# Optimization experiments

Measured on AMD Instinct MI355X. Metric: run time of the kernel, lower is better.

The kernel has to match this reference:

```python
import jax, jax.numpy as jnp
import numpy as np

D_MODEL = 1024
NUM_HEADS = 16
HEAD_DIM = D_MODEL // NUM_HEADS


def setup_inputs() -> dict:
    key = jax.random.key(0)
    ks = jax.random.split(key, 9)
    s = 1.0 / np.sqrt(D_MODEL)
    x = jax.random.normal(ks[0], (2, 2048, D_MODEL), dtype=jnp.float32)
    Wq = jax.random.uniform(ks[1], (D_MODEL, D_MODEL), jnp.float32, -s, s)
    bq = jax.random.uniform(ks[2], (D_MODEL,), jnp.float32, -s, s)
    Wk = jax.random.uniform(ks[3], (D_MODEL, D_MODEL), jnp.float32, -s, s)
    bk = jax.random.uniform(ks[4], (D_MODEL,), jnp.float32, -s, s)
    Wv = jax.random.uniform(ks[5], (D_MODEL, D_MODEL), jnp.float32, -s, s)
    bv = jax.random.uniform(ks[6], (D_MODEL,), jnp.float32, -s, s)
    Wo = jax.random.uniform(ks[7], (D_MODEL, D_MODEL), jnp.float32, -s, s)
    bo = jax.random.uniform(ks[8], (D_MODEL,), jnp.float32, -s, s)
    return {"x": x, "Wq": Wq, "bq": bq, "Wk": Wk, "bk": bk,
            "Wv": Wv, "bv": bv, "Wo": Wo, "bo": bo}


def reference(x, Wq, bq, Wk, bk, Wv, bv, Wo, bo):
    B, S, _ = x.shape
    def split_heads(t):  # [B,S,D] -> [B,H,S,hd]
        return t.reshape(B, S, NUM_HEADS, HEAD_DIM).transpose(0, 2, 1, 3)
    q = split_heads(x @ Wq + bq)
    k = split_heads(x @ Wk + bk)
    v = split_heads(x @ Wv + bv)
    scores = jnp.einsum('bhqd,bhkd->bhqk', q, k) / np.sqrt(HEAD_DIM)
    attn = jax.nn.softmax(scores, axis=-1)
    ctx = jnp.einsum('bhqk,bhkd->bhqd', attn, v)
    ctx = ctx.transpose(0, 2, 1, 3).reshape(B, S, D_MODEL)
    return ctx @ Wo + bo
```

## Files before the change

### kernel.cpp

```cpp
#include <hip/hip_runtime.h>
#include <stdint.h>

#define DM 1024
#define SEQ 2048
#define NTOK 4096
#define HD 64

typedef __bf16 bf16x8 __attribute__((ext_vector_type(8)));
typedef float f32x4 __attribute__((ext_vector_type(4)));
typedef uint32_t u32x2 __attribute__((ext_vector_type(2)));
typedef uint32_t u32x4 __attribute__((ext_vector_type(4)));

#if __has_builtin(__builtin_amdgcn_exp2f)
#define EXP2F(x) __builtin_amdgcn_exp2f(x)
#else
#define EXP2F(x) exp2f(x)
#endif

__device__ __forceinline__ void gll16f(const char* g, char* lds_wave_base, int lane) {
#if __has_builtin(__builtin_amdgcn_global_load_lds)
  __builtin_amdgcn_global_load_lds(
      (const __attribute__((address_space(1))) void*)g,
      (__attribute__((address_space(3))) void*)lds_wave_base, 16, 0, 0);
#else
  *(bf16x8*)(lds_wave_base + lane * 16) = *(const bf16x8*)g;
#endif
}

__device__ __forceinline__ uint16_t f2bf(float f) {
  uint32_t x = __float_as_uint(f);
  return (uint16_t)((x + 0x7fffu + ((x >> 16) & 1u)) >> 16);
}

__device__ __forceinline__ uint32_t cvtpk(float a, float b) {
  uint32_t r;
  asm("v_cvt_pk_bf16_f32 %0, %1, %2" : "=v"(r) : "v"(a), "v"(b));
  return r;
}

__device__ __forceinline__ bf16x8 mk8(uint32_t a, uint32_t b, uint32_t c, uint32_t d) {
  u32x4 t = {a, b, c, d};
  return __builtin_bit_cast(bf16x8, t);
}

__global__ void cvt_x_kernel(const float* __restrict__ x, uint16_t* __restrict__ xb) {
  int i = (blockIdx.x * 256 + threadIdx.x) * 4;
  float4 v = *(const float4*)&x[i];
  uint64_t pk = (uint64_t)f2bf(v.x) | ((uint64_t)f2bf(v.y) << 16) |
                ((uint64_t)f2bf(v.z) << 32) | ((uint64_t)f2bf(v.w) << 48);
  *(uint64_t*)&xb[i] = pk;
}

__global__ void twt4_kernel(const float* __restrict__ W0, const float* __restrict__ W1,
                            const float* __restrict__ W2, const float* __restrict__ W3,
                            uint16_t* __restrict__ T0, uint16_t* __restrict__ T1,
                            uint16_t* __restrict__ T2, uint16_t* __restrict__ T3) {
  __shared__ float t[32][33];
  int z = blockIdx.z;
  const float* W = (z == 0) ? W0 : (z == 1) ? W1 : (z == 2) ? W2 : W3;
  uint16_t* T = (z == 0) ? T0 : (z == 1) ? T1 : (z == 2) ? T2 : T3;
  int tx = threadIdx.x, ty = threadIdx.y;
  int kb = blockIdx.y * 32, nb = blockIdx.x * 32;
#pragma unroll
  for (int i = 0; i < 4; i++)
    t[ty + i * 8][tx] = W[(kb + ty + i * 8) * DM + nb + tx];
  __syncthreads();
#pragma unroll
  for (int i = 0; i < 4; i++)
    T[(nb + ty + i * 8) * DM + kb + tx] = f2bf(t[tx][ty + i * 8]);
}

template <int MODE, int MF>
__device__ __forceinline__ void gemm_body(const uint16_t* __restrict__ A,
                                          const uint16_t* __restrict__ Bt,
                                          const float* __restrict__ bias, float scale,
                                          void* __restrict__ out, uint16_t* lds) {
  const int tid = threadIdx.x;
  const int w = tid >> 6, lane = tid & 63;
  const int wr = w >> 1, wc = w & 1;
  const int a15 = lane & 15, a4 = lane >> 4;
  const int m0 = blockIdx.y * (MF * 32), n0 = blockIdx.x * 128;
  uint16_t* lgA = lds;
  uint16_t* lgB = lds + MF * 1024;
  f32x4 acc[MF][4];
#pragma unroll
  for (int m = 0; m < MF; m++)
#pragma unroll
    for (int n = 0; n < 4; n++) acc[m][n] = (f32x4){0.f, 0.f, 0.f, 0.f};

  const char* Ag = (const char*)(A + (size_t)m0 * DM);
  const char* Bg = (const char*)(Bt + (size_t)n0 * DM);

  for (int k0 = 0; k0 < DM; k0 += 32) {
#pragma unroll
    for (int c = 0; c < MF / 2; c++) {
      int o = w * (MF * 512) + c * 1024 + lane * 16;
      int row = o >> 6, colb = o & 63;
      gll16f(Ag + (size_t)row * (DM * 2) + k0 * 2 + colb,
             (char*)lgA + w * (MF * 512) + c * 1024, lane);
    }
#pragma unroll
    for (int c = 0; c < 2; c++) {
      int o = w * 2048 + c * 1024 + lane * 16;
      int row = o >> 6, colb = o & 63;
      gll16f(Bg + (size_t)row * (DM * 2) + k0 * 2 + colb,
             (char*)lgB + w * 2048 + c * 1024, lane);
    }
    __syncthreads();
    bf16x8 af[MF], bfr[4];
#pragma unroll
    for (int m = 0; m < MF; m++)
      af[m] = *(const bf16x8*)&lgA[(wr * (MF * 16) + m * 16 + a15) * 32 + a4 * 8];
#pragma unroll
    for (int n = 0; n < 4; n++)
      bfr[n] = *(const bf16x8*)&lgB[(wc * 64 + n * 16 + a15) * 32 + a4 * 8];
#pragma unroll
    for (int m = 0; m < MF; m++)
#pragma unroll
      for (int n = 0; n < 4; n++)
        acc[m][n] = __builtin_amdgcn_mfma_f32_16x16x32_bf16(af[m], bfr[n], acc[m][n], 0, 0, 0);
    __syncthreads();
  }

#pragma unroll
  for (int m = 0; m < MF; m++) {
#pragma unroll
    for (int n = 0; n < 4; n++) {
      int gr0 = m0 + wr * (MF * 16) + m * 16 + a4 * 4;
      int col = n0 + wc * 64 + n * 16 + a15;
      float bv = bias[col];
      if constexpr (MODE == 2) {
        float* O = (float*)out;
#pragma unroll
        for (int j = 0; j < 4; j++)
          O[(size_t)(gr0 + j) * DM + col] = acc[m][n][j] + bv;
      } else if constexpr (MODE == 0) {
        uint16_t* O = (uint16_t*)out;
        int h = col >> 6, d = col & 63;
#pragma unroll
        for (int j = 0; j < 4; j++) {
          int gr = gr0 + j;
          int b = gr >> 11, s = gr & 2047;
          O[((size_t)(((b << 4) + h)) * SEQ + s) * HD + d] = f2bf((acc[m][n][j] + bv) * scale);
        }
      } else {
        uint16_t* O = (uint16_t*)out;
        int h = col >> 6, d = col & 63;
        int b = gr0 >> 11, s0 = gr0 & 2047;
        uint64_t pk = 0;
#pragma unroll
        for (int j = 0; j < 4; j++)
          pk |= (uint64_t)f2bf(acc[m][n][j] + bv) << (16 * j);
        *(uint64_t*)&O[((size_t)(((b << 4) + h)) * HD + d) * SEQ + s0] = pk;
      }
    }
  }
}

#define CS_SCALE 0.180336880f

__global__ __launch_bounds__(256, 2) void gemm_qkv_kernel(
    const uint16_t* __restrict__ xb, const uint16_t* __restrict__ wtq,
    const uint16_t* __restrict__ wtk, const uint16_t* __restrict__ wtv,
    const float* __restrict__ bq, const float* __restrict__ bk,
    const float* __restrict__ bv, uint16_t* __restrict__ qo,
    uint16_t* __restrict__ ko, uint16_t* __restrict__ vto) {
  __shared__ __attribute__((aligned(16))) uint16_t lds[2 * 128 * 32];
  int z = blockIdx.z;
  if (z == 0)      gemm_body<0, 4>(xb, wtq, bq, CS_SCALE, qo, lds);
  else if (z == 1) gemm_body<0, 4>(xb, wtk, bk, 1.0f, ko, lds);
  else             gemm_body<1, 4>(xb, wtv, bv, 1.0f, vto, lds);
}

__global__ __launch_bounds__(256, 2) void gemm_out_kernel(
    const uint16_t* __restrict__ ctx, const uint16_t* __restrict__ wto,
    const float* __restrict__ bo, float* __restrict__ out) {
  __shared__ __attribute__((aligned(16))) uint16_t lds[2 * 1024 + 128 * 32];
  gemm_body<2, 2>(ctx, wto, bo, 1.0f, out, lds);
}

__global__ __launch_bounds__(256, 2) void attn_kernel(
    const uint16_t* __restrict__ qg, const uint16_t* __restrict__ kg,
    const uint16_t* __restrict__ vtg, uint16_t* __restrict__ ctx) {
  const int tid = threadIdx.x;
  const int w = tid >> 6, l = tid & 63;
  const int l15 = l & 15, g = l >> 4;
  int id = blockIdx.x;
  int wg = (id & 7) * 64 + (id >> 3);
  int bh = wg >> 4, qb = wg & 15;
  const int q0 = qb * 128 + w * 32;
  const uint16_t* Qb = qg + (size_t)bh * SEQ * HD;
  const char* Kc = (const char*)(kg + (size_t)bh * SEQ * HD);
  const char* Vc = (const char*)(vtg + (size_t)bh * HD * SEQ);

  __shared__ __attribute__((aligned(16))) char Klds[2][8192];
  __shared__ __attribute__((aligned(16))) char Vlds[2][8192];

  const int srow = l >> 3;
  const int scolx = ((l & 7) * 16) ^ (srow << 4);

#define STAGE(BI, IT)                                                          \
  {                                                                            \
    const int it1_ = (IT);                                                     \
    _Pragma("unroll") for (int i = 0; i < 2; i++) {                            \
      int r = w * 16 + i * 8 + srow;                                           \
      gll16f(Kc + (size_t)(it1_ * 64 + r) * 128 + scolx,                       \
             &Klds[BI][w * 2048 + i * 1024], l);                               \
      gll16f(Vc + (size_t)r * (SEQ * 2) + it1_ * 128 + scolx,                  \
             &Vlds[BI][w * 2048 + i * 1024], l);                               \
    }                                                                          \
  }

  bf16x8 bq[2][2];
#pragma unroll
  for (int qs = 0; qs < 2; qs++)
#pragma unroll
    for (int ks = 0; ks < 2; ks++)
      bq[qs][ks] = *(const bf16x8*)&Qb[(size_t)(q0 + qs * 16 + l15) * HD + ks * 32 + g * 8];

  f32x4 o[4][2];
#pragma unroll
  for (int dt = 0; dt < 4; dt++)
#pragma unroll
    for (int qs = 0; qs < 2; qs++) o[dt][qs] = (f32x4){0.f, 0.f, 0.f, 0.f};
  f32x4 ol0 = {0.f, 0.f, 0.f, 0.f}, ol1 = {0.f, 0.f, 0.f, 0.f};
  const int swz = (l15 & 7) << 4;
  const uint32_t ONE2 = 0x3F803F80u;
  const bf16x8 aones = mk8(ONE2, ONE2, ONE2, ONE2);

  STAGE(0, 0);

#define ATTN_TILE(IT, BI, BN)                                                  \
  {                                                                            \
    const int it_ = (IT);                                                      \
    if (it_ + 1 < SEQ / 64) {                                                  \
      STAGE(BN, it_ + 1);                                                      \
      asm volatile("s_waitcnt vmcnt(4)\n\ts_barrier" ::: "memory");            \
    } else {                                                                   \
      asm volatile("s_waitcnt vmcnt(0)\n\ts_barrier" ::: "memory");            \
    }                                                                          \
                                            \
    bf16x8 ak[4][2];                                                           \
    _Pragma("unroll") for (int kt = 0; kt < 4; kt++)                           \
        _Pragma("unroll") for (int ks = 0; ks < 2; ks++)                       \
            ak[kt][ks] = *(const bf16x8*)&Klds[BI][(kt * 16 + l15) * 128 +     \
                                                   ((ks * 64 + g * 16) ^ swz)];\
      \
    bf16x8 av[4][2];                                                           \
    _Pragma("unroll") for (int dt = 0; dt < 4; dt++)                           \
        _Pragma("unroll") for (int kb = 0; kb < 2; kb++) {                     \
      int rb = (dt * 16 + l15) * 128;                                          \
      u32x2 aa = *(const u32x2*)&Vlds[BI][rb + ((kb * 64 + g * 8) ^ swz)];     \
      u32x2 bb = *(const u32x2*)&Vlds[BI][rb + ((kb * 64 + g * 8 + 32) ^ swz)];\
      av[dt][kb] = mk8(aa[0], aa[1], bb[0], bb[1]);                            \
    }                                                                          \
                                           \
    f32x4 s[2][4];                                                             \
    _Pragma("unroll") for (int qs = 0; qs < 2; qs++)                           \
        _Pragma("unroll") for (int kt = 0; kt < 4; kt++)                       \
            s[qs][kt] = (f32x4){0.f, 0.f, 0.f, 0.f};                           \
    __builtin_amdgcn_s_setprio(1);                                             \
    _Pragma("unroll") for (int kt = 0; kt < 4; kt++)                           \
        _Pragma("unroll") for (int ks = 0; ks < 2; ks++) {                     \
      s[0][kt] = __builtin_amdgcn_mfma_f32_16x16x32_bf16(ak[kt][ks], bq[0][ks], s[0][kt], 0, 0, 0); \
      s[1][kt] = __builtin_amdgcn_mfma_f32_16x16x32_bf16(ak[kt][ks], bq[1][ks], s[1][kt], 0, 0, 0); \
    }                                                                          \
    __builtin_amdgcn_s_setprio(0);                                             \
        \
    float p0[4][4], p1[4][4];                                                  \
    _Pragma("unroll") for (int kt = 0; kt < 4; kt++)                           \
        _Pragma("unroll") for (int j = 0; j < 4; j++) {                        \
      p0[kt][j] = EXP2F(s[0][kt][j]);                                          \
      p1[kt][j] = EXP2F(s[1][kt][j]);                                          \
    }                                                                          \
    bf16x8 bp0[2], bp1[2];                                                     \
    _Pragma("unroll") for (int kb = 0; kb < 2; kb++) {                         \
      bp0[kb] = mk8(cvtpk(p0[2 * kb][0], p0[2 * kb][1]),                       \
                    cvtpk(p0[2 * kb][2], p0[2 * kb][3]),                       \
                    cvtpk(p0[2 * kb + 1][0], p0[2 * kb + 1][1]),               \
                    cvtpk(p0[2 * kb + 1][2], p0[2 * kb + 1][3]));              \
      bp1[kb] = mk8(cvtpk(p1[2 * kb][0], p1[2 * kb][1]),                       \
                    cvtpk(p1[2 * kb][2], p1[2 * kb][3]),                       \
                    cvtpk(p1[2 * kb + 1][0], p1[2 * kb + 1][1]),               \
                    cvtpk(p1[2 * kb + 1][2], p1[2 * kb + 1][3]));              \
    }                                                                          \
                                                \
    __builtin_amdgcn_s_setprio(1);                                             \
    _Pragma("unroll") for (int dt = 0; dt < 4; dt++)                           \
        _Pragma("unroll") for (int kb = 0; kb < 2; kb++) {                     \
      o[dt][0] = __builtin_amdgcn_mfma_f32_16x16x32_bf16(av[dt][kb], bp0[kb], o[dt][0], 0, 0, 0); \
      o[dt][1] = __builtin_amdgcn_mfma_f32_16x16x32_bf16(av[dt][kb], bp1[kb], o[dt][1], 0, 0, 0); \
    }                                                                          \
    _Pragma("unroll") for (int kb = 0; kb < 2; kb++) {                         \
      ol0 = __builtin_amdgcn_mfma_f32_16x16x32_bf16(aones, bp0[kb], ol0, 0, 0, 0); \
      ol1 = __builtin_amdgcn_mfma_f32_16x16x32_bf16(aones, bp1[kb], ol1, 0, 0, 0); \
    }                                                                          \
    __builtin_amdgcn_s_setprio(0);                                             \
    asm volatile("s_waitcnt lgkmcnt(0)\n\ts_barrier" ::: "memory");            \
  }

  for (int it2 = 0; it2 < SEQ / 128; ++it2) {
    ATTN_TILE(2 * it2, 0, 1);
    ATTN_TILE(2 * it2 + 1, 1, 0);
  }
#undef ATTN_TILE
#undef STAGE

  float inv0 = 1.0f / ol0[0];
  float inv1 = 1.0f / ol1[0];
  int b = bh >> 4, h = bh & 15;
  uint16_t* cr0 = ctx + (size_t)(b * SEQ + q0 + l15) * DM + h * HD + 4 * g;
  uint16_t* cr1 = cr0 + (size_t)16 * DM;
#pragma unroll
  for (int dt = 0; dt < 4; dt++) {
    u32x2 wv;
    wv[0] = cvtpk(o[dt][0][0] * inv0, o[dt][0][1] * inv0);
    wv[1] = cvtpk(o[dt][0][2] * inv0, o[dt][0][3] * inv0);
    *(u32x2*)&cr0[dt * 16] = wv;
    u32x2 wv2;
    wv2[0] = cvtpk(o[dt][1][0] * inv1, o[dt][1][1] * inv1);
    wv2[1] = cvtpk(o[dt][1][2] * inv1, o[dt][1][3] * inv1);
    *(u32x2*)&cr1[dt * 16] = wv2;
  }
}

extern "C" void kernel_launch(void* const* d_in, const int* in_sizes, int n_in,
                              void* d_out, int out_size, void* d_ws, size_t ws_size,
                              hipStream_t stream) {
  const float* x  = (const float*)d_in[0];
  const float* Wq = (const float*)d_in[1];
  const float* bq = (const float*)d_in[2];
  const float* Wk = (const float*)d_in[3];
  const float* bk = (const float*)d_in[4];
  const float* Wv = (const float*)d_in[5];
  const float* bv = (const float*)d_in[6];
  const float* Wo = (const float*)d_in[7];
  const float* bo = (const float*)d_in[8];

  char* ws = (char*)d_ws;
  uint16_t* xb  = (uint16_t*)(ws);
  uint16_t* wtq = (uint16_t*)(ws + 8388608);
  uint16_t* wtk = (uint16_t*)(ws + 10485760);
  uint16_t* wtv = (uint16_t*)(ws + 12582912);
  uint16_t* wto = (uint16_t*)(ws + 14680064);
  uint16_t* qb  = (uint16_t*)(ws + 16777216);
  uint16_t* kb  = (uint16_t*)(ws + 25165824);
  uint16_t* vtb = (uint16_t*)(ws + 33554432);
  uint16_t* ctx = xb;

  cvt_x_kernel<<<dim3(4096), dim3(256), 0, stream>>>(x, xb);
  twt4_kernel<<<dim3(32, 32, 4), dim3(32, 8), 0, stream>>>(
      Wq, Wk, Wv, Wo, wtq, wtk, wtv, wto);
  gemm_qkv_kernel<<<dim3(8, 32, 3), dim3(256), 0, stream>>>(
      xb, wtq, wtk, wtv, bq, bk, bv, qb, kb, vtb);
  attn_kernel<<<dim3(512), dim3(256), 0, stream>>>(qb, kb, vtb, ctx);
  gemm_out_kernel<<<dim3(8, 64), dim3(256), 0, stream>>>(ctx, wto, bo, (float*)d_out);
}
```

Baseline: 109.5 us.

## Double GEMM K-step to 64 with XOR-swizzled LDS and pre-permuted V layout

The projection GEMMs now stage 64-wide K tiles instead of 32, using an XOR swizzle on the LDS column so fragment reads avoid bank conflicts, and issue two MFMA k-substeps per barrier pair. The V-transpose output of the QKV GEMM is written in a permuted order within each 64-token chunk, which lets the attention kernel load V fragments with a single 16-byte LDS read instead of two 8-byte reads plus a repack. This halves the number of barriers in the GEMM loop but doubles LDS usage per block, which may limit occupancy.

After: 96.08 us. 12.3% less time.

```diff
diff --git a/kernel.cpp b/kernel.cpp
--- a/kernel.cpp
+++ b/kernel.cpp
@@ -80,8 +80,8 @@
   const int wr = w >> 1, wc = w & 1;
   const int a15 = lane & 15, a4 = lane >> 4;
   const int m0 = blockIdx.y * (MF * 32), n0 = blockIdx.x * 128;
-  uint16_t* lgA = lds;
-  uint16_t* lgB = lds + MF * 1024;
+  char* lgA = (char*)lds;
+  char* lgB = (char*)(lds + MF * 2048);
   f32x4 acc[MF][4];
 #pragma unroll
   for (int m = 0; m < MF; m++)
@@ -90,35 +90,43 @@
 
   const char* Ag = (const char*)(A + (size_t)m0 * DM);
   const char* Bg = (const char*)(Bt + (size_t)n0 * DM);
-
-  for (int k0 = 0; k0 < DM; k0 += 32) {
-#pragma unroll
-    for (int c = 0; c < MF / 2; c++) {
-      int o = w * (MF * 512) + c * 1024 + lane * 16;
-      int row = o >> 6, colb = o & 63;
-      gll16f(Ag + (size_t)row * (DM * 2) + k0 * 2 + colb,
-             (char*)lgA + w * (MF * 512) + c * 1024, lane);
+  const int srow = lane >> 3;
+  const int scol = ((lane & 7) * 16) ^ (srow << 4);
+  const int swz = (a15 & 7) << 4;
+
+  for (int k0 = 0; k0 < DM; k0 += 64) {
+#pragma unroll
+    for (int c = 0; c < MF; c++) {
+      int ro = w * (MF * 8) + c * 8 + srow;
+      gll16f(Ag + (size_t)ro * (DM * 2) + k0 * 2 + scol, lgA + (w * MF + c) * 1024, lane);
     }
 #pragma unroll
-    for (int c = 0; c < 2; c++) {
-      int o = w * 2048 + c * 1024 + lane * 16;
-      int row = o >> 6, colb = o & 63;
-      gll16f(Bg + (size_t)row * (DM * 2) + k0 * 2 + colb,
-             (char*)lgB + w * 2048 + c * 1024, lane);
+    for (int c = 0; c < 4; c++) {
+      int ro = w * 32 + c * 8 + srow;
+      gll16f(Bg + (size_t)ro * (DM * 2) + k0 * 2 + scol, lgB + (w * 4 + c) * 1024, lane);
     }
     __syncthreads();
-    bf16x8 af[MF], bfr[4];
+    bf16x8 af[MF][2], bfr[4][2];
 #pragma unroll
     for (int m = 0; m < MF; m++)
-      af[m] = *(const bf16x8*)&lgA[(wr * (MF * 16) + m * 16 + a15) * 32 + a4 * 8];
+#pragma unroll
+      for (int kk = 0; kk < 2; kk++)
+        af[m][kk] = *(const bf16x8*)(lgA + (wr * (MF * 16) + m * 16 + a15) * 128 +
+                                     ((kk * 64 + a4 * 16) ^ swz));
 #pragma unroll
     for (int n = 0; n < 4; n++)
-      bfr[n] = *(const bf16x8*)&lgB[(wc * 64 + n * 16 + a15) * 32 + a4 * 8];
-#pragma unroll
-    for (int m = 0; m < MF; m++)
-#pragma unroll
-      for (int n = 0; n < 4; n++)
-        acc[m][n] = __builtin_amdgcn_mfma_f32_16x16x32_bf16(af[m], bfr[n], acc[m][n], 0, 0, 0);
+#pragma unroll
+      for (int kk = 0; kk < 2; kk++)
+        bfr[n][kk] = *(const bf16x8*)(lgB + (wc * 64 + n * 16 + a15) * 128 +
+                                      ((kk * 64 + a4 * 16) ^ swz));
+#pragma unroll
+    for (int kk = 0; kk < 2; kk++)
+#pragma unroll
+      for (int m = 0; m < MF; m++)
+#pragma unroll
+        for (int n = 0; n < 4; n++)
+          acc[m][n] = __builtin_amdgcn_mfma_f32_16x16x32_bf16(af[m][kk], bfr[n][kk],
+                                                              acc[m][n], 0, 0, 0);
     __syncthreads();
   }
 
@@ -147,11 +155,13 @@
         uint16_t* O = (uint16_t*)out;
         int h = col >> 6, d = col & 63;
         int b = gr0 >> 11, s0 = gr0 & 2047;
+        int it = s0 >> 6, s6 = s0 & 63;
+        int pos = (s6 >> 5) * 32 + ((s6 >> 2) & 3) * 8 + ((s6 >> 4) & 1) * 4;
         uint64_t pk = 0;
 #pragma unroll
         for (int j = 0; j < 4; j++)
           pk |= (uint64_t)f2bf(acc[m][n][j] + bv) << (16 * j);
-        *(uint64_t*)&O[((size_t)(((b << 4) + h)) * HD + d) * SEQ + s0] = pk;
+        *(uint64_t*)&O[((size_t)(((b << 4) + h)) * HD + d) * SEQ + it * 64 + pos] = pk;
       }
     }
   }
@@ -165,7 +175,7 @@
     const float* __restrict__ bq, const float* __restrict__ bk,
     const float* __restrict__ bv, uint16_t* __restrict__ qo,
     uint16_t* __restrict__ ko, uint16_t* __restrict__ vto) {
-  __shared__ __attribute__((aligned(16))) uint16_t lds[2 * 128 * 32];
+  __shared__ __attribute__((aligned(16))) uint16_t lds[16384];
   int z = blockIdx.z;
   if (z == 0)      gemm_body<0, 4>(xb, wtq, bq, CS_SCALE, qo, lds);
   else if (z == 1) gemm_body<0, 4>(xb, wtk, bk, 1.0f, ko, lds);
@@ -175,7 +185,7 @@
 __global__ __launch_bounds__(256, 2) void gemm_out_kernel(
     const uint16_t* __restrict__ ctx, const uint16_t* __restrict__ wto,
     const float* __restrict__ bo, float* __restrict__ out) {
-  __shared__ __attribute__((aligned(16))) uint16_t lds[2 * 1024 + 128 * 32];
+  __shared__ __attribute__((aligned(16))) uint16_t lds[12288];
   gemm_body<2, 2>(ctx, wto, bo, 1.0f, out, lds);
 }
 
@@ -245,15 +255,12 @@
         _Pragma("unroll") for (int ks = 0; ks < 2; ks++)                       \
             ak[kt][ks] = *(const bf16x8*)&Klds[BI][(kt * 16 + l15) * 128 +     \
                                                    ((ks * 64 + g * 16) ^ swz)];\
-      \
+                     \
     bf16x8 av[4][2];                                                           \
     _Pragma("unroll") for (int dt = 0; dt < 4; dt++)                           \
-        _Pragma("unroll") for (int kb = 0; kb < 2; kb++) {                     \
-      int rb = (dt * 16 + l15) * 128;                                          \
-      u32x2 aa = *(const u32x2*)&Vlds[BI][rb + ((kb * 64 + g * 8) ^ swz)];     \
-      u32x2 bb = *(const u32x2*)&Vlds[BI][rb + ((kb * 64 + g * 8 + 32) ^ swz)];\
-      av[dt][kb] = mk8(aa[0], aa[1], bb[0], bb[1]);                            \
-    }                                                                          \
+        _Pragma("unroll") for (int kb = 0; kb < 2; kb++)                       \
+            av[dt][kb] = *(const bf16x8*)&Vlds[BI][(dt * 16 + l15) * 128 +     \
+                                                   ((kb * 64 + g * 16) ^ swz)];\
                                            \
     f32x4 s[2][4];                                                             \
     _Pragma("unroll") for (int qs = 0; qs < 2; qs++)                           \
```
